# Performance work log

Hardware: AMD Instinct MI355X
Metric: run time of the kernel (lower is better)

Reference implementation:

```python
import jax, jax.numpy as jnp
import numpy as np
from jax import lax

ALPHA = 0.1
HIDDEN_DIM = 512


def setup_inputs() -> dict:
    key = jax.random.key(0)
    ks = jax.random.split(key, 8)
    B, T, I, H, O, R = 64, 1024, 128, 512, 512, 2
    x = jax.random.normal(ks[0], (B, T, I), dtype=jnp.float32)
    h0 = jnp.zeros((B, H), dtype=jnp.float32)
    Wxh = jax.random.normal(ks[1], (H, I), dtype=jnp.float32) / np.sqrt(I)
    bxh = jax.random.normal(ks[2], (H,), dtype=jnp.float32) * 0.01
    U = jax.random.normal(ks[3], (H, R), dtype=jnp.float32) / np.sqrt(H)
    V = jax.random.normal(ks[4], (H, R), dtype=jnp.float32) / np.sqrt(H)
    Why = jax.random.normal(ks[5], (O, H), dtype=jnp.float32) / np.sqrt(H)
    bhy = jax.random.normal(ks[6], (O,), dtype=jnp.float32) * 0.01
    return {"x": x, "h0": h0, "Wxh": Wxh, "bxh": bxh, "U": U, "V": V,
            "Why": Why, "bhy": bhy}


def reference(x, h0, Wxh, bxh, U, V, Why, bhy):
    # x: (B,T,I); precompute the input projection for all timesteps at once
    xproj = jnp.einsum('bti,hi->bth', x, Wxh) + bxh  # (B,T,H)

    def step(h, xp_t):
        # low-rank recurrent map: h @ V @ U.T / hidden_dim
        pre = xp_t + (h @ V) @ U.T / HIDDEN_DIM  # (B,H)
        h_new = (1.0 - ALPHA) * h + ALPHA * jnp.tanh(pre)
        return h_new, h_new

    _, hs = lax.scan(step, h0, jnp.swapaxes(xproj, 0, 1))  # hs: (T,B,H)
    h_all = jnp.swapaxes(hs, 0, 1)  # (B,T,H)
    y = jnp.einsum('bth,oh->bto', h_all, Why) + bhy  # (B,T,O)
    return y, h_all
```

## Files before the change

### kernel.cpp

```cpp
#include <hip/hip_runtime.h>
#include <hip/hip_bf16.h>
#include <cstdint>

#define B_ 64
#define T_ 1024
#define I_ 128
#define H_ 512
#define O_ 512

#define CHUNK_L 64
#define NCHUNK (T_ / CHUNK_L)
#define WARM_ 96

typedef short bf16x8 __attribute__((ext_vector_type(8)));
typedef float f32x4 __attribute__((ext_vector_type(4)));

typedef const __attribute__((address_space(1))) void* gptr_t;
typedef __attribute__((address_space(3))) void* lptr_t;

__device__ __forceinline__ unsigned short f2bf(float f) {
    unsigned int u = __float_as_uint(f);
    u += 0x7fffu + ((u >> 16) & 1u);
    return (unsigned short)(u >> 16);
}
__device__ __forceinline__ float bf2f(unsigned short b) {
    return __uint_as_float(((unsigned int)b) << 16);
}
__device__ __forceinline__ float fast_tanh(float x) {
    float e = __builtin_amdgcn_exp2f(x * 2.8853900817779268f);
    return 1.0f - 2.0f * __builtin_amdgcn_rcpf(e + 1.0f);
}

template <int CTRL>
__device__ __forceinline__ float dpp_add(float v) {
    int t = __builtin_amdgcn_update_dpp(0, __float_as_int(v), CTRL, 0xf, 0xf, true);
    return v + __int_as_float(t);
}
__device__ __forceinline__ float wave_sum64(float v) {
    v = dpp_add<0x111>(v);
    v = dpp_add<0x112>(v);
    v = dpp_add<0x114>(v);
    v = dpp_add<0x118>(v);
    v = dpp_add<0x142>(v);
    v = dpp_add<0x143>(v);
    return __uint_as_float(__builtin_amdgcn_readlane(__float_as_uint(v), 63));
}

#define NX_ (B_ * T_ * I_)
#define NW_ (H_ * I_)
#define NY_ (O_ * H_)

__global__ __launch_bounds__(256)
void cast_all(const float* __restrict__ x, const float* __restrict__ Wxh,
              const float* __restrict__ Why, unsigned short* __restrict__ xb,
              unsigned short* __restrict__ wb, unsigned short* __restrict__ yb) {
    int i4 = (blockIdx.x * 256 + threadIdx.x) * 4;
    const float* s;
    unsigned short* d;
    int off;
    if (i4 < NX_)             { s = x;   d = xb; off = i4; }
    else if (i4 < NX_ + NW_)  { s = Wxh; d = wb; off = i4 - NX_; }
    else                      { s = Why; d = yb; off = i4 - NX_ - NW_; }
    float4 v = *(const float4*)(s + off);
    ushort4 o;
    o.x = f2bf(v.x); o.y = f2bf(v.y); o.z = f2bf(v.z); o.w = f2bf(v.w);
    *(ushort4*)(d + off) = o;
}

#define CPAD_F32 140
#define CPAD_BF16 136

template <bool STORE_BF16>
__global__ __launch_bounds__(256)
void gemm_bt(const unsigned short* __restrict__ A,
             const unsigned short* __restrict__ Bm,
             const float* __restrict__ bias,
             void* __restrict__ Cout,
             int M, int N, int K) {
    __shared__ unsigned short As[128 * 32];
    __shared__ unsigned short Bs[128 * 32];
    __shared__ __align__(16) unsigned char cbuf_raw[32 * CPAD_F32 * 4];

    const int tid  = threadIdx.x;
    const int lane = tid & 63;
    const int w    = tid >> 6;
    const int wm   = (w >> 1) * 64;
    const int wn   = (w & 1) * 64;
    const int nblk = N >> 7;
    const int bm   = (int)(blockIdx.x / nblk) << 7;
    const int bn   = (int)(blockIdx.x % nblk) << 7;

    f32x4 acc[4][4] = {};

    const int srow = tid >> 2;
    const int scol = (tid & 3) << 3;
    const unsigned short* gA0 = A  + (size_t)(bm + srow) * K + scol;
    const unsigned short* gA1 = A  + (size_t)(bm + 64 + srow) * K + scol;
    const unsigned short* gB0 = Bm + (size_t)(bn + srow) * K + scol;
    const unsigned short* gB1 = Bm + (size_t)(bn + 64 + srow) * K + scol;

    unsigned short* ldsA0 = As + w * 512;
    unsigned short* ldsA1 = As + 2048 + w * 512;
    unsigned short* ldsB0 = Bs + w * 512;
    unsigned short* ldsB1 = Bs + 2048 + w * 512;

    const int frow = lane & 15;
    const int fk   = (lane >> 4) << 3;

    for (int kt = 0; kt < K; kt += 32) {
        __syncthreads();
        __builtin_amdgcn_global_load_lds((gptr_t)(gA0 + kt), (lptr_t)ldsA0, 16, 0, 0);
        __builtin_amdgcn_global_load_lds((gptr_t)(gA1 + kt), (lptr_t)ldsA1, 16, 0, 0);
        __builtin_amdgcn_global_load_lds((gptr_t)(gB0 + kt), (lptr_t)ldsB0, 16, 0, 0);
        __builtin_amdgcn_global_load_lds((gptr_t)(gB1 + kt), (lptr_t)ldsB1, 16, 0, 0);
        __syncthreads();

        bf16x8 af[4], bf[4];
#pragma unroll
        for (int mt = 0; mt < 4; ++mt)
            af[mt] = *(const bf16x8*)(As + (wm + mt * 16 + frow) * 32 + fk);
#pragma unroll
        for (int nt = 0; nt < 4; ++nt)
            bf[nt] = *(const bf16x8*)(Bs + (wn + nt * 16 + frow) * 32 + fk);
#pragma unroll
        for (int mt = 0; mt < 4; ++mt)
#pragma unroll
            for (int nt = 0; nt < 4; ++nt)
                acc[mt][nt] = __builtin_amdgcn_mfma_f32_16x16x32_bf16(
                    af[mt], bf[nt], acc[mt][nt], 0, 0, 0);
    }

    const int c_col = lane & 15;
    const int c_row = (lane >> 4) << 2;
    const int slab  = (w >> 1) << 4;
    float* cbf = (float*)cbuf_raw;
    unsigned short* cbh = (unsigned short*)cbuf_raw;

#pragma unroll
    for (int mt = 0; mt < 4; ++mt) {
        __syncthreads();
        if (STORE_BF16) {
#pragma unroll
            for (int nt = 0; nt < 4; ++nt) {
                const int col = wn + nt * 16 + c_col;
                const float bv = bias[bn + col];
#pragma unroll
                for (int r = 0; r < 4; ++r)
                    cbh[(slab + c_row + r) * CPAD_BF16 + col] = f2bf(acc[mt][nt][r] + bv);
            }
        } else {
#pragma unroll
            for (int nt = 0; nt < 4; ++nt) {
                const int col = wn + nt * 16 + c_col;
                const float bv = bias[bn + col];
#pragma unroll
                for (int r = 0; r < 4; ++r)
                    cbf[(slab + c_row + r) * CPAD_F32 + col] = acc[mt][nt][r] + bv;
            }
        }
        __syncthreads();
        if (STORE_BF16) {
#pragma unroll
            for (int p = 0; p < 2; ++p) {
                const int lrow = (tid >> 4) + p * 16;
                const int colg = (tid & 15) * 8;
                const int grow = bm + (lrow >> 4) * 64 + mt * 16 + (lrow & 15);
                uint4 vv = *(const uint4*)(cbh + lrow * CPAD_BF16 + colg);
                *(uint4*)((unsigned short*)Cout + (size_t)grow * N + bn + colg) = vv;
            }
        } else {
#pragma unroll
            for (int p = 0; p < 4; ++p) {
                const int lrow = (tid >> 5) + p * 8;
                const int col4 = (tid & 31) * 4;
                const int grow = bm + (lrow >> 4) * 64 + mt * 16 + (lrow & 15);
                float4 vv = *(const float4*)(cbf + lrow * CPAD_F32 + col4);
                *(float4*)((float*)Cout + (size_t)grow * N + bn + col4) = vv;
            }
        }
    }
}

__global__ __launch_bounds__(64)
void scan_kernel(const unsigned short* __restrict__ xproj,
                 const float* __restrict__ h0,
                 const float* __restrict__ U,
                 const float* __restrict__ V,
                 float* __restrict__ hall_f32,
                 unsigned short* __restrict__ hall_bf) {
    const int blk = blockIdx.x;
    const int b = blk / NCHUNK;
    const int c = blk % NCHUNK;
    const int t_start = c * CHUNK_L;
    const int t0 = (t_start - WARM_ > 0) ? (t_start - WARM_) : 0;
    const int nwarm = t_start - t0;
    const int NT = nwarm + CHUNK_L;

    const int lane = threadIdx.x;
    const int hbase = lane * 8;

    const float inv_h = 1.0f / (float)H_;
    float h[8], V0[8], V1[8], U0[8], U1[8];
#pragma unroll
    for (int j = 0; j < 8; ++j) {
        V0[j] = V[(hbase + j) * 2 + 0] * inv_h;
        V1[j] = V[(hbase + j) * 2 + 1] * inv_h;
        U0[j] = U[(hbase + j) * 2 + 0];
        U1[j] = U[(hbase + j) * 2 + 1];
    }
    if (t0 == 0) {
#pragma unroll
        for (int j = 0; j < 8; ++j) h[j] = h0[b * H_ + hbase + j];
    } else {
#pragma unroll
        for (int j = 0; j < 8; ++j) h[j] = 0.f;
    }

    const unsigned short* xp = xproj + ((size_t)b * T_ + t0) * H_ + hbase;
    float* ho = hall_f32 + (size_t)b * T_ * H_ + hbase;
    unsigned short* hb = hall_bf + (size_t)b * T_ * H_ + hbase;

    float s0 = 0.f, s1 = 0.f;
    if (t0 == 0) {
        float a0 = 0.f, a1 = 0.f;
#pragma unroll
        for (int j = 0; j < 8; ++j) { a0 += h[j] * V0[j]; a1 += h[j] * V1[j]; }
        s0 = wave_sum64(a0);
        s1 = wave_sum64(a1);
    }

    uint4 xq0, xq1, xq2, xq3;
#define LOADX(DST, IDX)                                                        \
    {                                                                          \
        int _ii = (IDX);                                                       \
        _ii = _ii < NT ? _ii : NT - 1;                                         \
        DST = *(const uint4*)(xp + (size_t)_ii * H_);                          \
    }
    LOADX(xq0, 0)
    LOADX(xq1, 1)
    LOADX(xq2, 2)
    LOADX(xq3, 3)

#define SCAN_SLOT(REG, IDX, DO_STORE)                                          \
    {                                                                          \
        uint4 xc = REG;                                                        \
        LOADX(REG, (IDX) + 4)                                                  \
        float xp8[8];                                                          \
        {                                                                      \
            unsigned int uu[4] = {xc.x, xc.y, xc.z, xc.w};                     \
            _Pragma("unroll")                                                  \
            for (int q = 0; q < 4; ++q) {                                      \
                xp8[2 * q + 0] = bf2f((unsigned short)(uu[q] & 0xffffu));      \
                xp8[2 * q + 1] = bf2f((unsigned short)(uu[q] >> 16));          \
            }                                                                  \
        }                                                                      \
        float g[8];                                                            \
        _Pragma("unroll")                                                      \
        for (int j = 0; j < 8; ++j)                                            \
            g[j] = fast_tanh(xp8[j] + s0 * U0[j] + s1 * U1[j]);                \
        _Pragma("unroll")                                                      \
        for (int j = 0; j < 8; ++j)                                            \
            h[j] = 0.9f * h[j] + 0.1f * g[j];                                  \
        float p0a = 0.f, p0b = 0.f, p1a = 0.f, p1b = 0.f;                      \
        _Pragma("unroll")                                                      \
        for (int j = 0; j < 4; ++j) {                                          \
            p0a += g[j] * V0[j];       p0b += g[j + 4] * V0[j + 4];            \
            p1a += g[j] * V1[j];       p1b += g[j + 4] * V1[j + 4];            \
        }                                                                      \
        float r0 = wave_sum64(p0a + p0b);                                      \
        float r1 = wave_sum64(p1a + p1b);                                      \
        s0 = 0.9f * s0 + 0.1f * r0;                                            \
        s1 = 0.9f * s1 + 0.1f * r1;                                            \
        if (DO_STORE) {                                                        \
            const size_t tt = (size_t)(t0 + (IDX));                            \
            float4 v0 = make_float4(h[0], h[1], h[2], h[3]);                   \
            float4 v1 = make_float4(h[4], h[5], h[6], h[7]);                   \
            *(float4*)(ho + tt * H_ + 0) = v0;                                 \
            *(float4*)(ho + tt * H_ + 4) = v1;                                 \
            uint4 pb;                                                          \
            pb.x = ((unsigned int)f2bf(h[1]) << 16) | f2bf(h[0]);              \
            pb.y = ((unsigned int)f2bf(h[3]) << 16) | f2bf(h[2]);              \
            pb.z = ((unsigned int)f2bf(h[5]) << 16) | f2bf(h[4]);              \
            pb.w = ((unsigned int)f2bf(h[7]) << 16) | f2bf(h[6]);              \
            *(uint4*)(hb + tt * H_) = pb;                                      \
        }                                                                      \
    }

    int I = 0;
    for (; I < nwarm; I += 4) {
        SCAN_SLOT(xq0, I + 0, false)
        SCAN_SLOT(xq1, I + 1, false)
        SCAN_SLOT(xq2, I + 2, false)
        SCAN_SLOT(xq3, I + 3, false)
    }
    for (; I < NT; I += 4) {
        SCAN_SLOT(xq0, I + 0, true)
        SCAN_SLOT(xq1, I + 1, true)
        SCAN_SLOT(xq2, I + 2, true)
        SCAN_SLOT(xq3, I + 3, true)
    }
#undef SCAN_SLOT
#undef LOADX
}

extern "C" void kernel_launch(void* const* d_in, const int* in_sizes, int n_in,
                              void* d_out, int out_size, void* d_ws, size_t ws_size,
                              hipStream_t stream) {
    const float* x   = (const float*)d_in[0];
    const float* h0  = (const float*)d_in[1];
    const float* Wxh = (const float*)d_in[2];
    const float* bxh = (const float*)d_in[3];
    const float* U   = (const float*)d_in[4];
    const float* V   = (const float*)d_in[5];
    const float* Why = (const float*)d_in[6];
    const float* bhy = (const float*)d_in[7];

    float* y    = (float*)d_out;
    float* hall = y + (size_t)B_ * T_ * O_;

    unsigned short* x_bf    = (unsigned short*)d_ws;
    unsigned short* Wxh_bf  = x_bf + (size_t)B_ * T_ * I_;
    unsigned short* Why_bf  = Wxh_bf + (size_t)H_ * I_;
    unsigned short* xp_bf   = Why_bf + (size_t)O_ * H_;
    unsigned short* hall_bf = xp_bf + (size_t)B_ * T_ * H_;

    cast_all<<<(NX_ + NW_ + NY_) / 1024, 256, 0, stream>>>(
        x, Wxh, Why, x_bf, Wxh_bf, Why_bf);

    gemm_bt<true><<<dim3((B_ * T_ / 128) * (H_ / 128)), 256, 0, stream>>>(
        x_bf, Wxh_bf, bxh, xp_bf, B_ * T_, H_, I_);

    scan_kernel<<<B_ * NCHUNK, 64, 0, stream>>>(xp_bf, h0, U, V, hall, hall_bf);

    gemm_bt<false><<<dim3((B_ * T_ / 128) * (O_ / 128)), 256, 0, stream>>>(
        hall_bf, Why_bf, bhy, y, B_ * T_, O_, H_);
}
```

Measured before the change: 452.7 us.

## Double-buffer GEMM LDS tiles and halve recurrence chunk length

The bf16 GEMM now double-buffers its A/B tiles in shared memory. The next k-tile is issued via global_load_lds while MFMAs run on the current one, which leaves a single barrier per iteration. The epilogue staging buffer aliases the same shared allocation, so LDS footprint stays bounded. Separately, the recurrence chunk length drops from 64 to 32, doubling the number of chunks for more parallelism at the cost of more warmup overhead per chunk. The single barrier placed after compute may rely on the async LDS loads completing in time, which is a correctness risk.

Result: no change. 458.0 us (+1.2%).

```diff
diff --git a/kernel.cpp b/kernel.cpp
--- a/kernel.cpp
+++ b/kernel.cpp
@@ -8,7 +8,7 @@
 #define H_ 512
 #define O_ 512
 
-#define CHUNK_L 64
+#define CHUNK_L 32
 #define NCHUNK (T_ / CHUNK_L)
 #define WARM_ 96
 
@@ -77,9 +77,9 @@
              const float* __restrict__ bias,
              void* __restrict__ Cout,
              int M, int N, int K) {
-    __shared__ unsigned short As[128 * 32];
-    __shared__ unsigned short Bs[128 * 32];
-    __shared__ __align__(16) unsigned char cbuf_raw[32 * CPAD_F32 * 4];
+    __shared__ __align__(16) unsigned char smem_raw[32768];
+    unsigned short* As = (unsigned short*)smem_raw;
+    unsigned short* Bs = As + 8192;
 
     const int tid  = threadIdx.x;
     const int lane = tid & 63;
@@ -106,35 +106,49 @@
 
     const int frow = lane & 15;
     const int fk   = (lane >> 4) << 3;
-
-    for (int kt = 0; kt < K; kt += 32) {
-        __syncthreads();
-        __builtin_amdgcn_global_load_lds((gptr_t)(gA0 + kt), (lptr_t)ldsA0, 16, 0, 0);
-        __builtin_amdgcn_global_load_lds((gptr_t)(gA1 + kt), (lptr_t)ldsA1, 16, 0, 0);
-        __builtin_amdgcn_global_load_lds((gptr_t)(gB0 + kt), (lptr_t)ldsB0, 16, 0, 0);
-        __builtin_amdgcn_global_load_lds((gptr_t)(gB1 + kt), (lptr_t)ldsB1, 16, 0, 0);
-        __syncthreads();
-
+    const int nk   = K >> 5;
+
+#define STAGE_T(BUF, KT)                                                                          \
+    {                                                                                             \
+        const int _o = (BUF) * 4096;                                                              \
+        __builtin_amdgcn_global_load_lds((gptr_t)(gA0 + (KT)), (lptr_t)(ldsA0 + _o), 16, 0, 0);   \
+        __builtin_amdgcn_global_load_lds((gptr_t)(gA1 + (KT)), (lptr_t)(ldsA1 + _o), 16, 0, 0);   \
+        __builtin_amdgcn_global_load_lds((gptr_t)(gB0 + (KT)), (lptr_t)(ldsB0 + _o), 16, 0, 0);   \
+        __builtin_amdgcn_global_load_lds((gptr_t)(gB1 + (KT)), (lptr_t)(ldsB1 + _o), 16, 0, 0);   \
+    }
+
+    STAGE_T(0, 0)
+    __syncthreads();
+
+    for (int t = 0; t < nk; ++t) {
+        const int cur = t & 1;
+        if (t + 1 < nk) STAGE_T(cur ^ 1, (t + 1) << 5)
+
+        const unsigned short* Ab = As + cur * 4096;
+        const unsigned short* Bb = Bs + cur * 4096;
         bf16x8 af[4], bf[4];
 #pragma unroll
         for (int mt = 0; mt < 4; ++mt)
-            af[mt] = *(const bf16x8*)(As + (wm + mt * 16 + frow) * 32 + fk);
+            af[mt] = *(const bf16x8*)(Ab + (wm + mt * 16 + frow) * 32 + fk);
 #pragma unroll
         for (int nt = 0; nt < 4; ++nt)
-            bf[nt] = *(const bf16x8*)(Bs + (wn + nt * 16 + frow) * 32 + fk);
+            bf[nt] = *(const bf16x8*)(Bb + (wn + nt * 16 + frow) * 32 + fk);
 #pragma unroll
         for (int mt = 0; mt < 4; ++mt)
 #pragma unroll
             for (int nt = 0; nt < 4; ++nt)
                 acc[mt][nt] = __builtin_amdgcn_mfma_f32_16x16x32_bf16(
                     af[mt], bf[nt], acc[mt][nt], 0, 0, 0);
-    }
+
+        __syncthreads();
+    }
+#undef STAGE_T
 
     const int c_col = lane & 15;
     const int c_row = (lane >> 4) << 2;
     const int slab  = (w >> 1) << 4;
-    float* cbf = (float*)cbuf_raw;
-    unsigned short* cbh = (unsigned short*)cbuf_raw;
+    float* cbf = (float*)smem_raw;
+    unsigned short* cbh = (unsigned short*)smem_raw;
 
 #pragma unroll
     for (int mt = 0; mt < 4; ++mt) {
```
